# Optimization experiments

Hardware: AMD Instinct MI355X
Metric: run time of the kernel (lower is better)

Reference implementation:

```python
import jax, jax.numpy as jnp
import numpy as np

D_MODEL = 1024
NUM_HEADS = 16
HEAD_DIM = D_MODEL // NUM_HEADS
B, S = 2, 2048


def setup_inputs() -> dict:
    key = jax.random.key(0)
    ks = jax.random.split(key, 6)
    scale = 0.02
    return {
        "x": jax.random.normal(ks[0], (B, S, D_MODEL), dtype=jnp.float32),
        "mask": jax.random.normal(ks[1], (S, S), dtype=jnp.float32),
        "Wqkv": jax.random.normal(ks[2], (D_MODEL, 3 * D_MODEL), dtype=jnp.float32) * scale,
        "bqkv": jax.random.normal(ks[3], (3 * D_MODEL,), dtype=jnp.float32) * scale,
        "Wout": jax.random.normal(ks[4], (D_MODEL, D_MODEL), dtype=jnp.float32) * scale,
        "bout": jax.random.normal(ks[5], (D_MODEL,), dtype=jnp.float32) * scale,
    }


def reference(x, mask, Wqkv, bqkv, Wout, bout):
    b, s, d = x.shape
    h, hd = NUM_HEADS, HEAD_DIM
    qkv = x @ Wqkv + bqkv                              # [b, s, 3d]
    qkv = qkv.reshape(b, s, h, 3 * hd).transpose(0, 2, 1, 3)  # [b, h, s, 3hd]
    q, k, v = jnp.split(qkv, 3, axis=-1)               # each [b, h, s, hd]
    scaled = jnp.einsum("bhqd,bhkd->bhqk", q, k) / jnp.sqrt(jnp.float32(hd))
    scaled = scaled + mask                             # mask [s, s] broadcasts
    attn = jax.nn.softmax(scaled, axis=-1)
    values = jnp.einsum("bhqk,bhkd->bhqd", attn, v)    # [b, h, s, hd]
    values = values.transpose(0, 2, 1, 3).reshape(b, s, d)
    return values @ Wout + bout
```

## Files before the change

### kernel.cpp

```cpp
#include <hip/hip_runtime.h>
#include <hip/hip_bf16.h>

#define D_MODEL 1024
#define NH 16
#define HD 64
#define BATCH 2
#define SEQ 2048
#define M_TOTAL (BATCH*SEQ)

typedef _Float16 f16;
typedef _Float16 half8 __attribute__((ext_vector_type(8)));
typedef _Float16 half4v __attribute__((ext_vector_type(4)));
typedef float floatx4 __attribute__((ext_vector_type(4)));

__device__ inline void gload_lds16(const void* g, void* l) {
    __builtin_amdgcn_global_load_lds(
        (const __attribute__((address_space(1))) unsigned int*)g,
        (__attribute__((address_space(3))) unsigned int*)l, 16, 0, 0);
}

__global__ void cvt_f32_f16(const float* __restrict__ src, f16* __restrict__ dst, int n4) {
    int i = blockIdx.x * blockDim.x + threadIdx.x;
    if (i < n4) {
        float4 v = ((const float4*)src)[i];
        half4v o = { (f16)v.x, (f16)v.y, (f16)v.z, (f16)v.w };
        *(half4v*)(dst + (long)i * 4) = o;
    }
}

__global__ void exp_cvt(const float* __restrict__ src, f16* __restrict__ dst, int n4) {
    int i = blockIdx.x * blockDim.x + threadIdx.x;
    if (i < n4) {
        float4 v = ((const float4*)src)[i];
        half4v o = { (f16)__expf(v.x), (f16)__expf(v.y), (f16)__expf(v.z), (f16)__expf(v.w) };
        *(half4v*)(dst + (long)i * 4) = o;
    }
}

__global__ void transpose_cvt(const float* __restrict__ src, f16* __restrict__ dst, int R, int C) {
    __shared__ float tile[32][33];
    int tx = threadIdx.x;
    int ty = threadIdx.y;
    int c0 = blockIdx.x * 32;
    int r0 = blockIdx.y * 32;
    for (int yy = 0; yy < 32; yy += 8)
        tile[ty + yy][tx] = src[(long)(r0 + ty + yy) * C + c0 + tx];
    __syncthreads();
    for (int yy = 0; yy < 32; yy += 8)
        dst[(long)(c0 + ty + yy) * R + r0 + tx] = (f16)tile[tx][ty + yy];
}

template<int MODE, int TN>
__global__ __launch_bounds__(256) void gemm_mfma(
    const f16* __restrict__ A, const f16* __restrict__ BT,
    const float* __restrict__ bias,
    f16* __restrict__ Qh, f16* __restrict__ Kh, f16* __restrict__ Vtg,
    float* __restrict__ out, int Kdim)
{
    constexpr int NF = TN / 32;
    __shared__ f16 Ah[2][128 * 64];
    __shared__ f16 Bh[2][TN * 64];
    int tid  = threadIdx.x;
    int wid  = tid >> 6;
    int lane = tid & 63;
    int quad = lane >> 4;
    int l16  = lane & 15;
    int m0 = blockIdx.y * 128;
    int n0 = blockIdx.x * TN;
    int mrow = (wid >> 1) * 64;
    int ncol = (wid & 1) * (TN / 2);
    int grow = lane >> 3;
    int gchunk = (lane & 7) ^ (grow & 7);
    int sw0 = ((quad)     ^ (l16 & 7)) * 8;
    int sw1 = ((quad + 4) ^ (l16 & 7)) * 8;

    floatx4 acc[4][NF];
    #pragma unroll
    for (int mb = 0; mb < 4; mb++)
        #pragma unroll
        for (int nb = 0; nb < NF; nb++) acc[mb][nb] = (floatx4){0.f, 0.f, 0.f, 0.f};

    const f16* Abase = A + (long)m0 * Kdim;
    const f16* Bbase = BT + (long)n0 * Kdim;

    auto stage = [&](int buf, int k0) {
        #pragma unroll
        for (int j = 0; j < 4; j++) {
            int r = j * 32 + wid * 8 + grow;
            gload_lds16(Abase + (long)r * Kdim + k0 + gchunk * 8, &Ah[buf][(j * 32 + wid * 8) * 64]);
        }
        #pragma unroll
        for (int j = 0; j < TN / 32; j++) {
            int r = j * 32 + wid * 8 + grow;
            gload_lds16(Bbase + (long)r * Kdim + k0 + gchunk * 8, &Bh[buf][(j * 32 + wid * 8) * 64]);
        }
    };

    stage(0, 0);
    __syncthreads();
    int cur = 0;
    for (int k0 = 0; k0 < Kdim; k0 += 64) {
        if (k0 + 64 < Kdim) stage(cur ^ 1, k0 + 64);
        #pragma unroll
        for (int h = 0; h < 2; h++) {
            int sw = h ? sw1 : sw0;
            half8 af[4];
            #pragma unroll
            for (int mb = 0; mb < 4; mb++)
                af[mb] = *(const half8*)&Ah[cur][(mrow + mb * 16 + l16) * 64 + sw];
            #pragma unroll
            for (int nb = 0; nb < NF; nb++) {
                half8 bf = *(const half8*)&Bh[cur][(ncol + nb * 16 + l16) * 64 + sw];
                #pragma unroll
                for (int mb = 0; mb < 4; mb++)
                    acc[mb][nb] = __builtin_amdgcn_mfma_f32_16x16x32_f16(af[mb], bf, acc[mb][nb], 0, 0, 0);
            }
        }
        __syncthreads();
        cur ^= 1;
    }

    #pragma unroll
    for (int nb = 0; nb < NF; nb++) {
        int n = n0 + ncol + nb * 16 + l16;
        float bv = bias[n];
        int head = 0, t = 0, d = 0;
        if (MODE == 0) { head = n / 192; int rem = n % 192; t = rem / 64; d = rem % 64; }
        #pragma unroll
        for (int mb = 0; mb < 4; mb++) {
            int mbase = m0 + mrow + mb * 16 + quad * 4;
            if (MODE == 0) {
                int b = mbase >> 11;
                int s = mbase & 2047;
                long bh = b * NH + head;
                if (t == 2) {
                    half4v pack;
                    #pragma unroll
                    for (int r = 0; r < 4; r++) pack[r] = (f16)(acc[mb][nb][r] + bv);
                    *(half4v*)&Vtg[(bh * HD + d) * SEQ + s] = pack;
                } else if (t == 0) {
                    #pragma unroll
                    for (int r = 0; r < 4; r++)
                        Qh[(bh * SEQ + s + r) * HD + d] = (f16)((acc[mb][nb][r] + bv) * 0.125f);
                } else {
                    #pragma unroll
                    for (int r = 0; r < 4; r++)
                        Kh[(bh * SEQ + s + r) * HD + d] = (f16)(acc[mb][nb][r] + bv);
                }
            } else {
                #pragma unroll
                for (int r = 0; r < 4; r++)
                    out[(long)(mbase + r) * D_MODEL + n] = acc[mb][nb][r] + bv;
            }
        }
    }
}

__global__ __launch_bounds__(512) void attn(
    const f16* __restrict__ Qh, const f16* __restrict__ Kh, const f16* __restrict__ Vtg,
    const f16* __restrict__ E, f16* __restrict__ valh)
{
    __shared__ f16 Kl[64 * 64];
    __shared__ f16 Vt[64 * 64];
    __shared__ f16 El[128 * 64];
    __shared__ f16 Pl[8][16 * 68];
    int tid  = threadIdx.x;
    int wid  = tid >> 6;
    int lane = tid & 63;
    int quad = lane >> 4;
    int l16  = lane & 15;
    int bh = blockIdx.y;
    int b  = bh >> 4;
    int h  = bh & 15;
    int qblk = blockIdx.x * 128;
    int q0 = qblk + wid * 16;

    int wrow = wid * 8 + (lane >> 3);
    int kchunk = (lane & 7) ^ (wrow & 7);
    int sw0 = ((quad)     ^ (l16 & 7)) * 8;
    int sw1 = ((quad + 4) ^ (l16 & 7)) * 8;

    const f16* Qbase = Qh + ((long)bh * SEQ + q0) * HD;
    half8 qf[2];
    #pragma unroll
    for (int c = 0; c < 2; c++)
        qf[c] = *(const half8*)&Qbase[(long)l16 * HD + c * 32 + quad * 8];

    floatx4 Of[4];
    float sums[4];
    #pragma unroll
    for (int nb = 0; nb < 4; nb++) Of[nb] = (floatx4){0.f, 0.f, 0.f, 0.f};
    #pragma unroll
    for (int r = 0; r < 4; r++) sums[r] = 0.f;

    const f16* Kb = Kh + (long)bh * SEQ * HD;
    const f16* Vb = Vtg + (long)bh * HD * SEQ;
    const f16* Eb = E + (long)qblk * SEQ;

    for (int k0 = 0; k0 < SEQ; k0 += 64) {
        __syncthreads();
        gload_lds16(Kb + (long)(k0 + wrow) * HD + kchunk * 8, &Kl[(wid * 8) * 64]);
        gload_lds16(Vb + (long)wrow * SEQ + k0 + kchunk * 8, &Vt[(wid * 8) * 64]);
        gload_lds16(Eb + (long)wrow * SEQ + k0 + kchunk * 8, &El[(wid * 8) * 64]);
        gload_lds16(Eb + (long)(64 + wrow) * SEQ + k0 + kchunk * 8, &El[(64 + wid * 8) * 64]);
        __syncthreads();

        floatx4 sc[4];
        #pragma unroll
        for (int kb = 0; kb < 4; kb++) {
            half8 kf0 = *(const half8*)&Kl[(kb * 16 + l16) * 64 + sw0];
            half8 kf1 = *(const half8*)&Kl[(kb * 16 + l16) * 64 + sw1];
            floatx4 s = (floatx4){0.f, 0.f, 0.f, 0.f};
            s = __builtin_amdgcn_mfma_f32_16x16x32_f16(qf[0], kf0, s, 0, 0, 0);
            s = __builtin_amdgcn_mfma_f32_16x16x32_f16(qf[1], kf1, s, 0, 0, 0);
            sc[kb] = s;
        }

        int lrow = wid * 16 + quad * 4;
        #pragma unroll
        for (int kb = 0; kb < 4; kb++) {
            int cchunk = kb * 2 + (l16 >> 3);
            #pragma unroll
            for (int r = 0; r < 4; r++) {
                int lr = lrow + r;
                f16 ev = El[lr * 64 + ((cchunk ^ (lr & 7)) * 8) + (l16 & 7)];
                float p = (float)ev * __expf(sc[kb][r]);
                sums[r] += p;
                Pl[wid][(quad * 4 + r) * 68 + kb * 16 + l16] = (f16)p;
            }
        }

        half8 pf0 = *(const half8*)&Pl[wid][l16 * 68 + quad * 8];
        half8 pf1 = *(const half8*)&Pl[wid][l16 * 68 + 32 + quad * 8];

        #pragma unroll
        for (int nb = 0; nb < 4; nb++) {
            half8 vf0 = *(const half8*)&Vt[(nb * 16 + l16) * 64 + sw0];
            half8 vf1 = *(const half8*)&Vt[(nb * 16 + l16) * 64 + sw1];
            Of[nb] = __builtin_amdgcn_mfma_f32_16x16x32_f16(pf0, vf0, Of[nb], 0, 0, 0);
            Of[nb] = __builtin_amdgcn_mfma_f32_16x16x32_f16(pf1, vf1, Of[nb], 0, 0, 0);
        }
    }

    float rinv[4];
    #pragma unroll
    for (int r = 0; r < 4; r++) {
        float s = sums[r];
        s += __shfl_xor(s, 1);
        s += __shfl_xor(s, 2);
        s += __shfl_xor(s, 4);
        s += __shfl_xor(s, 8);
        rinv[r] = 1.f / s;
    }

    #pragma unroll
    for (int nb = 0; nb < 4; nb++)
        #pragma unroll
        for (int r = 0; r < 4; r++) {
            int q = q0 + quad * 4 + r;
            int d = nb * 16 + l16;
            valh[((long)(b * SEQ + q)) * D_MODEL + h * HD + d] = (f16)(Of[nb][r] * rinv[r]);
        }
}

extern "C" void kernel_launch(void* const* d_in, const int* in_sizes, int n_in,
                              void* d_out, int out_size, void* d_ws, size_t ws_size,
                              hipStream_t stream) {
    const float* x    = (const float*)d_in[0];
    const float* mask = (const float*)d_in[1];
    const float* Wqkv = (const float*)d_in[2];
    const float* bqkv = (const float*)d_in[3];
    const float* Wout = (const float*)d_in[4];
    const float* bout = (const float*)d_in[5];
    float* out = (float*)d_out;

    char* ws = (char*)d_ws;
    f16* xh    = (f16*)(ws + 0);
    f16* E     = (f16*)(ws + 0);
    f16* WqkvT = (f16*)(ws + 8388608);
    f16* WoutT = (f16*)(ws + 14680064);
    f16* Qh    = (f16*)(ws + 16777216);
    f16* Kh    = (f16*)(ws + 25165824);
    f16* Vtg   = (f16*)(ws + 33554432);
    f16* valh  = (f16*)(ws + 41943040);

    cvt_f32_f16<<<4096, 256, 0, stream>>>(x, xh, M_TOTAL * D_MODEL / 4);
    transpose_cvt<<<dim3(96, 32), dim3(32, 8), 0, stream>>>(Wqkv, WqkvT, 1024, 3072);
    transpose_cvt<<<dim3(32, 32), dim3(32, 8), 0, stream>>>(Wout, WoutT, 1024, 1024);
    gemm_mfma<0, 128><<<dim3(24, 32), 256, 0, stream>>>(xh, WqkvT, bqkv, Qh, Kh, Vtg, nullptr, 1024);
    exp_cvt<<<4096, 256, 0, stream>>>(mask, E, SEQ * SEQ / 4);
    attn<<<dim3(16, 32), 512, 0, stream>>>(Qh, Kh, Vtg, E, valh);
    gemm_mfma<1, 64><<<dim3(16, 32), 256, 0, stream>>>(valh, WoutT, bout, nullptr, nullptr, nullptr, out, 1024);
}
```

Measured before the change: 236.1 us.

## Double-buffer K/V in attention, load mask into registers, single-buffer GEMM

```diff
diff --git a/kernel.cpp b/kernel.cpp
--- a/kernel.cpp
+++ b/kernel.cpp
@@ -58,8 +58,8 @@
     float* __restrict__ out, int Kdim)
 {
     constexpr int NF = TN / 32;
-    __shared__ f16 Ah[2][128 * 64];
-    __shared__ f16 Bh[2][TN * 64];
+    __shared__ f16 Ah[128 * 64];
+    __shared__ f16 Bh[TN * 64];
     int tid  = threadIdx.x;
     int wid  = tid >> 6;
     int lane = tid & 63;
@@ -83,41 +83,34 @@
     const f16* Abase = A + (long)m0 * Kdim;
     const f16* Bbase = BT + (long)n0 * Kdim;
 
-    auto stage = [&](int buf, int k0) {
+    for (int k0 = 0; k0 < Kdim; k0 += 64) {
         #pragma unroll
         for (int j = 0; j < 4; j++) {
             int r = j * 32 + wid * 8 + grow;
-            gload_lds16(Abase + (long)r * Kdim + k0 + gchunk * 8, &Ah[buf][(j * 32 + wid * 8) * 64]);
+            gload_lds16(Abase + (long)r * Kdim + k0 + gchunk * 8, &Ah[(j * 32 + wid * 8) * 64]);
         }
         #pragma unroll
         for (int j = 0; j < TN / 32; j++) {
             int r = j * 32 + wid * 8 + grow;
-            gload_lds16(Bbase + (long)r * Kdim + k0 + gchunk * 8, &Bh[buf][(j * 32 + wid * 8) * 64]);
-        }
-    };
-
-    stage(0, 0);
-    __syncthreads();
-    int cur = 0;
-    for (int k0 = 0; k0 < Kdim; k0 += 64) {
-        if (k0 + 64 < Kdim) stage(cur ^ 1, k0 + 64);
+            gload_lds16(Bbase + (long)r * Kdim + k0 + gchunk * 8, &Bh[(j * 32 + wid * 8) * 64]);
+        }
+        __syncthreads();
         #pragma unroll
         for (int h = 0; h < 2; h++) {
             int sw = h ? sw1 : sw0;
             half8 af[4];
             #pragma unroll
             for (int mb = 0; mb < 4; mb++)
-                af[mb] = *(const half8*)&Ah[cur][(mrow + mb * 16 + l16) * 64 + sw];
+                af[mb] = *(const half8*)&Ah[(mrow + mb * 16 + l16) * 64 + sw];
             #pragma unroll
             for (int nb = 0; nb < NF; nb++) {
-                half8 bf = *(const half8*)&Bh[cur][(ncol + nb * 16 + l16) * 64 + sw];
+                half8 bf = *(const half8*)&Bh[(ncol + nb * 16 + l16) * 64 + sw];
                 #pragma unroll
                 for (int mb = 0; mb < 4; mb++)
                     acc[mb][nb] = __builtin_amdgcn_mfma_f32_16x16x32_f16(af[mb], bf, acc[mb][nb], 0, 0, 0);
             }
         }
         __syncthreads();
-        cur ^= 1;
     }
 
     #pragma unroll
@@ -160,9 +153,8 @@
     const f16* __restrict__ Qh, const f16* __restrict__ Kh, const f16* __restrict__ Vtg,
     const f16* __restrict__ E, f16* __restrict__ valh)
 {
-    __shared__ f16 Kl[64 * 64];
-    __shared__ f16 Vt[64 * 64];
-    __shared__ f16 El[128 * 64];
+    __shared__ f16 Kl[2][64 * 64];
+    __shared__ f16 Vt[2][64 * 64];
     __shared__ f16 Pl[8][16 * 68];
     int tid  = threadIdx.x;
     int wid  = tid >> 6;
@@ -197,49 +189,67 @@
     const f16* Vb = Vtg + (long)bh * HD * SEQ;
     const f16* Eb = E + (long)qblk * SEQ;
 
-    for (int k0 = 0; k0 < SEQ; k0 += 64) {
-        __syncthreads();
-        gload_lds16(Kb + (long)(k0 + wrow) * HD + kchunk * 8, &Kl[(wid * 8) * 64]);
-        gload_lds16(Vb + (long)wrow * SEQ + k0 + kchunk * 8, &Vt[(wid * 8) * 64]);
-        gload_lds16(Eb + (long)wrow * SEQ + k0 + kchunk * 8, &El[(wid * 8) * 64]);
-        gload_lds16(Eb + (long)(64 + wrow) * SEQ + k0 + kchunk * 8, &El[(64 + wid * 8) * 64]);
-        __syncthreads();
+    auto stage = [&](int buf, int k0) {
+        gload_lds16(Kb + (long)(k0 + wrow) * HD + kchunk * 8, &Kl[buf][(wid * 8) * 64]);
+        gload_lds16(Vb + (long)wrow * SEQ + k0 + kchunk * 8, &Vt[buf][(wid * 8) * 64]);
+    };
+    auto loadE = [&](f16 (&ef)[4][4], int k0) {
+        #pragma unroll
+        for (int r = 0; r < 4; r++) {
+            const f16* Erow = Eb + (long)(wid * 16 + quad * 4 + r) * SEQ + k0 + l16;
+            #pragma unroll
+            for (int kb = 0; kb < 4; kb++) ef[r][kb] = Erow[kb * 16];
+        }
+    };
+
+    f16 efA[4][4], efB[4][4];
+    stage(0, 0);
+    loadE(efA, 0);
+    __syncthreads();
+
+    auto iter = [&](const int buf, f16 (&efC)[4][4], f16 (&efN)[4][4], int k0) {
+        bool notlast = (k0 + 64 < SEQ);
+        if (notlast) stage(buf ^ 1, k0 + 64);
 
         floatx4 sc[4];
         #pragma unroll
         for (int kb = 0; kb < 4; kb++) {
-            half8 kf0 = *(const half8*)&Kl[(kb * 16 + l16) * 64 + sw0];
-            half8 kf1 = *(const half8*)&Kl[(kb * 16 + l16) * 64 + sw1];
+            half8 kf0 = *(const half8*)&Kl[buf][(kb * 16 + l16) * 64 + sw0];
+            half8 kf1 = *(const half8*)&Kl[buf][(kb * 16 + l16) * 64 + sw1];
             floatx4 s = (floatx4){0.f, 0.f, 0.f, 0.f};
             s = __builtin_amdgcn_mfma_f32_16x16x32_f16(qf[0], kf0, s, 0, 0, 0);
             s = __builtin_amdgcn_mfma_f32_16x16x32_f16(qf[1], kf1, s, 0, 0, 0);
             sc[kb] = s;
         }
 
-        int lrow = wid * 16 + quad * 4;
-        #pragma unroll
-        for (int kb = 0; kb < 4; kb++) {
-            int cchunk = kb * 2 + (l16 >> 3);
+        #pragma unroll
+        for (int kb = 0; kb < 4; kb++)
             #pragma unroll
             for (int r = 0; r < 4; r++) {
-                int lr = lrow + r;
-                f16 ev = El[lr * 64 + ((cchunk ^ (lr & 7)) * 8) + (l16 & 7)];
-                float p = (float)ev * __expf(sc[kb][r]);
+                float p = (float)efC[r][kb] * __expf(sc[kb][r]);
                 sums[r] += p;
                 Pl[wid][(quad * 4 + r) * 68 + kb * 16 + l16] = (f16)p;
             }
-        }
+
+        if (notlast) loadE(efN, k0 + 64);
 
         half8 pf0 = *(const half8*)&Pl[wid][l16 * 68 + quad * 8];
         half8 pf1 = *(const half8*)&Pl[wid][l16 * 68 + 32 + quad * 8];
 
         #pragma unroll
         for (int nb = 0; nb < 4; nb++) {
-            half8 vf0 = *(const half8*)&Vt[(nb * 16 + l16) * 64 + sw0];
-            half8 vf1 = *(const half8*)&Vt[(nb * 16 + l16) * 64 + sw1];
+            half8 vf0 = *(const half8*)&Vt[buf][(nb * 16 + l16) * 64 + sw0];
+            half8 vf1 = *(const half8*)&Vt[buf][(nb * 16 + l16) * 64 + sw1];
             Of[nb] = __builtin_amdgcn_mfma_f32_16x16x32_f16(pf0, vf0, Of[nb], 0, 0, 0);
             Of[nb] = __builtin_amdgcn_mfma_f32_16x16x32_f16(pf1, vf1, Of[nb], 0, 0, 0);
         }
+
+        __syncthreads();
+    };
+
+    for (int k0 = 0; k0 < SEQ; k0 += 128) {
+        iter(0, efA, efB, k0);
+        iter(1, efB, efA, k0 + 64);
     }
 
     float rinv[4];
```

After: 219.7 us. -6.9%, faster.
